# Performance work log

Measured on AMD Instinct MI355X. Metric: run time of the kernel, lower is better.

The kernel has to match this reference:

```python
import jax, jax.numpy as jnp
import numpy as np

TOK, CPC, RHY = 135, 12, 8
HID, STACK, KEY, EMB = 400, 32, 300, 50
B, T = 1, 4096


def setup_inputs() -> dict:
    key = jax.random.key(0)
    ks = jax.random.split(key, 32)
    w = lambda k, shape, s=0.05: jax.random.normal(k, shape, jnp.float32) * s
    inp = {
        'xr': jax.random.randint(ks[0], (B, T), 0, RHY, dtype=jnp.int32),
        'xcpc': jax.random.randint(ks[1], (B, T), 0, CPC, dtype=jnp.int32),
        'xma': jax.random.randint(ks[2], (B, T), 0, TOK, dtype=jnp.int32),
        'emb_midi': w(ks[3], (TOK, EMB)),
        'emb_cpc': w(ks[4], (CPC, EMB)),
        'emb_rhythm': w(ks[5], (RHY, EMB)),
        # note_rnn: 2-layer LSTM, input 3*EMB=150, hidden 400 (torch gate order i,f,g,o)
        'note_Wih0': w(ks[6], (4 * HID, 3 * EMB)),
        'note_Whh0': w(ks[7], (4 * HID, HID)),
        'note_bih0': w(ks[8], (4 * HID,)),
        'note_bhh0': w(ks[9], (4 * HID,)),
        'note_Wih1': w(ks[10], (4 * HID, HID)),
        'note_Whh1': w(ks[11], (4 * HID, HID)),
        'note_bih1': w(ks[12], (4 * HID,)),
        'note_bhh1': w(ks[13], (4 * HID,)),
        'note_fcW': w(ks[14], (3 * EMB, HID)),
        'note_fcb': w(ks[15], (3 * EMB,)),
        # stack memory
        'act_W': w(ks[16], (3, HID)),
        'act_b': w(ks[17], (3,)),
        'D_param': jax.random.normal(ks[18], (1, HID), jnp.float32),
        # key_rnn: 1-layer LSTM, input HID, hidden KEY
        'key_Wih': w(ks[19], (4 * KEY, HID)),
        'key_Whh': w(ks[20], (4 * KEY, KEY)),
        'key_bih': w(ks[21], (4 * KEY,)),
        'key_bhh': w(ks[22], (4 * KEY,)),
        'key_fcW': w(ks[23], (HID, KEY)),
        'key_fcb': w(ks[24], (HID,)),
    }
    return inp


def lstm_layer(x, Wih, Whh, bih, bhh):
    # x: [B,T,I] -> outputs [B,T,H], final (h,c) [B,H]. torch gate order i,f,g,o.
    Bsz = x.shape[0]
    H = Whh.shape[1]
    xg = jnp.einsum('bti,gi->btg', x, Wih) + bih  # precompute input projections

    def step(carry, xt):  # xt: [B,4H]
        h, c = carry
        g = xt + h @ Whh.T + bhh
        i, f, gg, o = jnp.split(g, 4, axis=-1)
        c = jax.nn.sigmoid(f) * c + jax.nn.sigmoid(i) * jnp.tanh(gg)
        h = jax.nn.sigmoid(o) * jnp.tanh(c)
        return (h, c), h

    init = (jnp.zeros((Bsz, H), x.dtype), jnp.zeros((Bsz, H), x.dtype))
    (h, c), hs = jax.lax.scan(step, init, jnp.swapaxes(xg, 0, 1))
    return jnp.swapaxes(hs, 0, 1), h, c


def stack_memory(rnn_out, act_W, act_b, D_param):
    # Per-timestep push/pop/no-op gated stack; returns per-step stack snapshots.
    Bsz, Tlen, H = rnn_out.shape
    probs = jax.nn.softmax(rnn_out @ act_W.T + act_b, axis=-1)            # [B,T,3]
    push_val = jax.nn.sigmoid(jnp.einsum('oh,bth->bt', D_param, rnn_out))  # [B,T]

    def step(s, xs):  # s: [B,STACK,H]
        p, pv = xs  # p: [B,3], pv: [B]
        a = jnp.concatenate([s[:, 1:], s[:, -1:]], axis=1)    # stack[:-1]=stack[1:]
        b = jnp.concatenate([a[:, :1], a[:, :-1]], axis=1)    # stack[1:]=stack[:-1]
        top = p[:, 0:1] * pv[:, None] + p[:, 1:2] * b[:, 1] + p[:, 2:3] * b[:, 0]
        s = b.at[:, 0].set(top)
        return s, s

    init = jnp.zeros((Bsz, STACK, H), rnn_out.dtype)
    _, stacks = jax.lax.scan(step, init, (jnp.swapaxes(probs, 0, 1), push_val.T))
    return jnp.swapaxes(stacks, 0, 1)  # [B,T,STACK,H]


def reference(xr, xcpc, xma, emb_midi, emb_cpc, emb_rhythm,
              note_Wih0, note_Whh0, note_bih0, note_bhh0,
              note_Wih1, note_Whh1, note_bih1, note_bhh1,
              note_fcW, note_fcb, act_W, act_b, D_param,
              key_Wih, key_Whh, key_bih, key_bhh, key_fcW, key_fcb):
    x = jnp.concatenate([emb_midi[xma], emb_cpc[xcpc], emb_rhythm[xr]], axis=2)  # [B,T,150]
    h0, _, _ = lstm_layer(x, note_Wih0, note_Whh0, note_bih0, note_bhh0)
    rnn_out, rh, rc = lstm_layer(h0, note_Wih1, note_Whh1, note_bih1, note_bhh1)
    rtoken_pred = rnn_out @ note_fcW.T + note_fcb  # dropout is identity in eval
    context = stack_memory(rnn_out, act_W, act_b, D_param)  # [B,T,STACK,HID]
    key_in = rh[:, None, :]  # [B,1,HID] (prev_key concat dropped; see notes)
    krnn_out, kh, kc = lstm_layer(key_in, key_Wih, key_Whh, key_bih, key_bhh)
    ktoken_pred = krnn_out @ key_fcW.T + key_fcb  # [B,1,HID]
    return (rtoken_pred, ktoken_pred, context)
```

## Files before the change

kernel.cpp:

```cpp
#include <hip/hip_runtime.h>
#include <stdint.h>

#define T_LEN 4096
#define HID   400
#define G4    1600
#define KDIM  300
#define STACKN 32

__device__ __forceinline__ float fsig(float x){ return 1.f/(1.f + __expf(-x)); }
__device__ __forceinline__ float ftanh(float x){ float e = __expf(2.f*x); return 1.f - 2.f/(e+1.f); }

__device__ __forceinline__ unsigned long long poll_u64(const unsigned long long* src, unsigned tag){
  unsigned long long x0 = __hip_atomic_load(src, __ATOMIC_RELAXED, __HIP_MEMORY_SCOPE_AGENT);
  unsigned long long x1 = __hip_atomic_load(src, __ATOMIC_RELAXED, __HIP_MEMORY_SCOPE_AGENT);
  unsigned long long x2 = __hip_atomic_load(src, __ATOMIC_RELAXED, __HIP_MEMORY_SCOPE_AGENT);
  unsigned long long x3 = __hip_atomic_load(src, __ATOMIC_RELAXED, __HIP_MEMORY_SCOPE_AGENT);
  while ((unsigned)(x0 >> 32) != tag){
    x0 = x1; x1 = x2; x2 = x3;
    x3 = __hip_atomic_load(src, __ATOMIC_RELAXED, __HIP_MEMORY_SCOPE_AGENT);
  }
  return x0;
}
__device__ __forceinline__ float poll_val(const unsigned long long* src, unsigned tag){
  union{unsigned u; float f;} cv; cv.u = (unsigned)poll_u64(src, tag);
  return cv.f;
}

__global__ void __launch_bounds__(256) kgemm0(
    const int* __restrict__ xma, const int* __restrict__ xcpc, const int* __restrict__ xr,
    const float* __restrict__ em, const float* __restrict__ ec, const float* __restrict__ er,
    const float* __restrict__ W, const float* __restrict__ b1, const float* __restrict__ b2,
    float* __restrict__ XG)
{
  __shared__ float xs[8*152];
  const int t0 = blockIdx.x*8;
  const int tid = threadIdx.x;
  for (int idx = tid; idx < 8*150; idx += 256){
    int tt = idx / 150, k = idx - tt*150;
    int t = t0 + tt;
    float v;
    if (k < 50)       v = em[(size_t)xma[t]*50 + k];
    else if (k < 100) v = ec[(size_t)xcpc[t]*50 + (k-50)];
    else              v = er[(size_t)xr[t]*50 + (k-100)];
    xs[tt*152 + k] = v;
  }
  __syncthreads();
  int r = blockIdx.y*256 + tid;
  if (r >= G4) return;
  float acc[8];
  #pragma unroll
  for (int i=0;i<8;i++) acc[i]=0.f;
  const float2* wr = (const float2*)(W + (size_t)r*150);
  for (int k2=0;k2<75;k2++){
    float2 w = wr[k2];
    int k = 2*k2;
    #pragma unroll
    for (int tt=0;tt<8;tt++)
      acc[tt] += w.x*xs[tt*152+k] + w.y*xs[tt*152+k+1];
  }
  float bb = b1[r] + b2[r];
  #pragma unroll
  for (int tt=0;tt<8;tt++)
    XG[(size_t)(t0+tt)*G4 + r] = acc[tt] + bb;
}

__global__ void __launch_bounds__(512,1) kpipe(
    const float* __restrict__ XG0,
    const float* __restrict__ Whh0, const float* __restrict__ Whh1,
    const float* __restrict__ Wih1, const float* __restrict__ bih1,
    const float* __restrict__ bhh1,
    float* __restrict__ RN,
    unsigned long long* hbufA, unsigned long long* hbufB,
    unsigned long long* gbuf, int T)
{
  const int role = blockIdx.x & 7;
  if (role > 2) return;
  const int sub = blockIdx.x >> 3;
  const int tid = threadIdx.x;
  const int row_local = tid >> 2;
  const int part = tid & 3;
  const bool mat = (tid < 400);
  const bool ew  = (tid >= 448 && tid < 473);
  const int  ej  = tid - 448;

  __shared__ float lds_h[HID];
  __shared__ float lds_g[100];

  if (role == 0){
    const int w = sub;
    float wreg[100];
    if (mat){
      int gate = row_local/25, jj = row_local%25;
      int row = gate*400 + w*25 + jj;
      const float4* wr = (const float4*)(Whh0 + (size_t)row*HID) + part*25;
      #pragma unroll
      for (int i=0;i<25;i++){
        float4 v = wr[i];
        wreg[4*i]=v.x; wreg[4*i+1]=v.y; wreg[4*i+2]=v.z; wreg[4*i+3]=v.w;
      }
    }
    const int j = w*25 + ej;
    float c = 0.f;
    for (int t=0; t<T; t++){
      float xgi=0.f, xgf=0.f, xgg=0.f, xgo=0.f;
      unsigned long long th0=0, th1=0, th2=0, th3=0;
      const unsigned long long* thp = 0;
      if (ew){
        const float* xrw = XG0 + (size_t)t*G4;
        xgi = xrw[j]; xgf = xrw[HID+j]; xgg = xrw[2*HID+j]; xgo = xrw[3*HID+j];
        if (t >= 7){
          thp = hbufB + (size_t)((t-6)&7)*HID + j;
          th0 = __hip_atomic_load(thp, __ATOMIC_RELAXED, __HIP_MEMORY_SCOPE_AGENT);
          th1 = __hip_atomic_load(thp, __ATOMIC_RELAXED, __HIP_MEMORY_SCOPE_AGENT);
          th2 = __hip_atomic_load(thp, __ATOMIC_RELAXED, __HIP_MEMORY_SCOPE_AGENT);
          th3 = __hip_atomic_load(thp, __ATOMIC_RELAXED, __HIP_MEMORY_SCOPE_AGENT);
        }
      }
      if (mat){
        float hv = 0.f;
        if (t > 0) hv = poll_val(hbufA + (size_t)(t&7)*HID + tid, (unsigned)t);
        lds_h[tid] = hv;
      }
      __syncthreads();
      float sum = 0.f;
      if (mat){
        const float4* hp = (const float4*)(lds_h + part*100);
        #pragma unroll
        for (int i=0;i<25;i++){
          float4 h4 = hp[i];
          sum += wreg[4*i]*h4.x + wreg[4*i+1]*h4.y + wreg[4*i+2]*h4.z + wreg[4*i+3]*h4.w;
        }
      }
      sum += __shfl_xor(sum, 1);
      sum += __shfl_xor(sum, 2);
      if (mat && part==0) lds_g[row_local] = sum;
      __syncthreads();
      if (ew){
        float gi = xgi + lds_g[ej];
        float gf = xgf + lds_g[25+ej];
        float gg = xgg + lds_g[50+ej];
        float go = xgo + lds_g[75+ej];
        float si = fsig(gi), sf = fsig(gf), so = fsig(go), tg = ftanh(gg);
        c = sf*c + si*tg;
        float h = so*ftanh(c);
        if (t >= 7){
          unsigned want = (unsigned)(t-6);
          while ((unsigned)(th0 >> 32) != want){
            th0 = th1; th1 = th2; th2 = th3;
            th3 = __hip_atomic_load(thp, __ATOMIC_RELAXED, __HIP_MEMORY_SCOPE_AGENT);
          }
        }
        union{unsigned u; float f;} cv; cv.f = h;
        unsigned long long pk = ((unsigned long long)(unsigned)(t+1) << 32) | (unsigned long long)cv.u;
        __hip_atomic_store(hbufA + (size_t)((t+1)&7)*HID + j, pk,
                           __ATOMIC_RELAXED, __HIP_MEMORY_SCOPE_AGENT);
      }
    }
  } else if (role == 1){
    const int f = sub;
    float wreg[100];
    float bias = 0.f;
    int grow = 0;
    if (mat){
      int gate = row_local/25, jj = row_local%25;
      grow = gate*400 + f*25 + jj;
      const float4* wr = (const float4*)(Wih1 + (size_t)grow*HID) + part*25;
      #pragma unroll
      for (int i=0;i<25;i++){
        float4 v = wr[i];
        wreg[4*i]=v.x; wreg[4*i+1]=v.y; wreg[4*i+2]=v.z; wreg[4*i+3]=v.w;
      }
      if (part==0) bias = bih1[grow] + bhh1[grow];
    }
    for (int t=0; t<T; t++){
      if (mat)
        lds_h[tid] = poll_val(hbufA + (size_t)((t+1)&7)*HID + tid, (unsigned)(t+1));
      __syncthreads();
      float sum = 0.f;
      if (mat){
        const float4* hp = (const float4*)(lds_h + part*100);
        #pragma unroll
        for (int i=0;i<25;i++){
          float4 h4 = hp[i];
          sum += wreg[4*i]*h4.x + wreg[4*i+1]*h4.y + wreg[4*i+2]*h4.z + wreg[4*i+3]*h4.w;
        }
      }
      sum += __shfl_xor(sum, 1);
      sum += __shfl_xor(sum, 2);
      if (mat && part==0){
        union{unsigned u; float f;} cv; cv.f = sum + bias;
        unsigned long long pk = ((unsigned long long)(unsigned)(t+1) << 32) | (unsigned long long)cv.u;
        __hip_atomic_store(gbuf + (size_t)((t+1)&7)*G4 + grow, pk,
                           __ATOMIC_RELAXED, __HIP_MEMORY_SCOPE_AGENT);
      }
      __syncthreads();
    }
  } else {
    const int l = sub;
    float wreg[100];
    if (mat){
      int gate = row_local/25, jj = row_local%25;
      int row = gate*400 + l*25 + jj;
      const float4* wr = (const float4*)(Whh1 + (size_t)row*HID) + part*25;
      #pragma unroll
      for (int i=0;i<25;i++){
        float4 v = wr[i];
        wreg[4*i]=v.x; wreg[4*i+1]=v.y; wreg[4*i+2]=v.z; wreg[4*i+3]=v.w;
      }
    }
    const int j = l*25 + ej;
    float c = 0.f;
    for (int t=0; t<T; t++){
      if (mat){
        float hv = 0.f;
        if (t > 0) hv = poll_val(hbufB + (size_t)(t&7)*HID + tid, (unsigned)t);
        lds_h[tid] = hv;
      }
      __syncthreads();
      float xg0=0.f, xg1v=0.f, xg2=0.f, xg3=0.f;
      if (ew){
        const unsigned long long* gb = gbuf + (size_t)((t+1)&7)*G4 + j;
        unsigned want = (unsigned)(t+1);
        unsigned long long v0, v1, v2, v3;
        for (;;){
          v0 = __hip_atomic_load(gb,        __ATOMIC_RELAXED, __HIP_MEMORY_SCOPE_AGENT);
          v1 = __hip_atomic_load(gb + 400,  __ATOMIC_RELAXED, __HIP_MEMORY_SCOPE_AGENT);
          v2 = __hip_atomic_load(gb + 800,  __ATOMIC_RELAXED, __HIP_MEMORY_SCOPE_AGENT);
          v3 = __hip_atomic_load(gb + 1200, __ATOMIC_RELAXED, __HIP_MEMORY_SCOPE_AGENT);
          if (((unsigned)(v0>>32)==want) & ((unsigned)(v1>>32)==want) &
              ((unsigned)(v2>>32)==want) & ((unsigned)(v3>>32)==want)) break;
        }
        union{unsigned u; float f;} c0,c1,c2,c3;
        c0.u=(unsigned)v0; c1.u=(unsigned)v1; c2.u=(unsigned)v2; c3.u=(unsigned)v3;
        xg0=c0.f; xg1v=c1.f; xg2=c2.f; xg3=c3.f;
      }
      float sum = 0.f;
      if (mat){
        const float4* hp = (const float4*)(lds_h + part*100);
        #pragma unroll
        for (int i=0;i<25;i++){
          float4 h4 = hp[i];
          sum += wreg[4*i]*h4.x + wreg[4*i+1]*h4.y + wreg[4*i+2]*h4.z + wreg[4*i+3]*h4.w;
        }
      }
      sum += __shfl_xor(sum, 1);
      sum += __shfl_xor(sum, 2);
      if (mat && part==0) lds_g[row_local] = sum;
      __syncthreads();
      if (ew){
        float gi = xg0  + lds_g[ej];
        float gf = xg1v + lds_g[25+ej];
        float gg = xg2  + lds_g[50+ej];
        float go = xg3  + lds_g[75+ej];
        float si = fsig(gi), sf = fsig(gf), so = fsig(go), tg = ftanh(gg);
        c = sf*c + si*tg;
        float h = so*ftanh(c);
        union{unsigned u; float f;} cv; cv.f = h;
        unsigned long long pk = ((unsigned long long)(unsigned)(t+1) << 32) | (unsigned long long)cv.u;
        __hip_atomic_store(hbufB + (size_t)((t+1)&7)*HID + j, pk,
                           __ATOMIC_RELAXED, __HIP_MEMORY_SCOPE_AGENT);
        RN[(size_t)t*HID + j] = h;
      }
    }
  }
}

__global__ void __launch_bounds__(256) krtoken(
    const float* __restrict__ RN, const float* __restrict__ fcW,
    const float* __restrict__ fcb, float* __restrict__ out)
{
  __shared__ float xs[8*400];
  const int t0 = blockIdx.x*8;
  const int tid = threadIdx.x;
  for (int idx = tid; idx < 8*400; idx += 256)
    xs[idx] = RN[(size_t)t0*400 + idx];
  __syncthreads();
  if (tid >= 150) return;
  float acc[8];
  #pragma unroll
  for (int i=0;i<8;i++) acc[i]=0.f;
  const float4* wr = (const float4*)(fcW + (size_t)tid*400);
  for (int k4=0;k4<100;k4++){
    float4 w = wr[k4];
    #pragma unroll
    for (int tt=0;tt<8;tt++){
      const float4 x4 = *(const float4*)(xs + tt*400 + 4*k4);
      acc[tt] += w.x*x4.x + w.y*x4.y + w.z*x4.z + w.w*x4.w;
    }
  }
  float bb = fcb[tid];
  #pragma unroll
  for (int tt=0;tt<8;tt++)
    out[(size_t)(t0+tt)*150 + tid] = acc[tt] + bb;
}

__global__ void kfinal(const float* __restrict__ RN, const float* __restrict__ actW,
                       const float* __restrict__ actb, const float* __restrict__ Dp,
                       float* __restrict__ vbuf)
{
  int t = blockIdx.x, l = threadIdx.x;
  const float* r = RN + (size_t)t*HID;
  float s0=0.f, s1=0.f, s2=0.f, sd=0.f;
  for (int k=l; k<HID; k+=64){
    float rv = r[k];
    s0 += actW[k]*rv;
    s1 += actW[400+k]*rv;
    s2 += actW[800+k]*rv;
    sd += Dp[k]*rv;
  }
  #pragma unroll
  for (int o=1;o<64;o<<=1){
    s0 += __shfl_xor(s0,o); s1 += __shfl_xor(s1,o);
    s2 += __shfl_xor(s2,o); sd += __shfl_xor(sd,o);
  }
  if (l==0){
    s0 += actb[0]; s1 += actb[1]; s2 += actb[2];
    float m = fmaxf(s0, fmaxf(s1, s2));
    float e0 = __expf(s0-m), e1 = __expf(s1-m), e2 = __expf(s2-m);
    float p0 = e0/(e0+e1+e2);
    vbuf[t] = p0 * fsig(sd);
  }
}

__global__ void kctx(const float* __restrict__ vbuf, uint4* __restrict__ ctx, int n16){
  int i = blockIdx.x*256 + threadIdx.x;
  int stride = gridDim.x*256;
  for (; i<n16; i+=stride){
    int t = i / 3200;
    int p = i - t*3200;
    uint4 z;
    if (p < 100){
      float v = vbuf[t];
      union{float f; uint32_t u;} cv; cv.f = v;
      z.x = z.y = z.z = z.w = cv.u;
    } else {
      z.x = z.y = z.z = z.w = 0u;
    }
    ctx[i] = z;
  }
}

__global__ void __launch_bounds__(512) kkey(
    const float* __restrict__ RN, const float* __restrict__ Wih,
    const float* __restrict__ bih, const float* __restrict__ bhh,
    const float* __restrict__ fcW, const float* __restrict__ fcb,
    float* __restrict__ out)
{
  __shared__ float rh[HID];
  __shared__ float gk[4*KDIM];
  __shared__ float hk[KDIM];
  int tid = threadIdx.x;
  if (tid < HID) rh[tid] = RN[(size_t)(T_LEN-1)*HID + tid];
  __syncthreads();
  for (int r = tid; r < 4*KDIM; r += 512){
    const float4* wr = (const float4*)(Wih + (size_t)r*HID);
    float acc = 0.f;
    for (int k4=0;k4<100;k4++){
      float4 w = wr[k4];
      const float4 x4 = *(const float4*)(rh + 4*k4);
      acc += w.x*x4.x + w.y*x4.y + w.z*x4.z + w.w*x4.w;
    }
    gk[r] = acc + bih[r] + bhh[r];
  }
  __syncthreads();
  if (tid < KDIM){
    float gi = gk[tid], gg = gk[2*KDIM+tid], go = gk[3*KDIM+tid];
    float cc = fsig(gi)*ftanh(gg);
    hk[tid] = fsig(go)*ftanh(cc);
  }
  __syncthreads();
  if (tid < HID){
    const float4* wr = (const float4*)(fcW + (size_t)tid*KDIM);
    float acc = 0.f;
    for (int k4=0;k4<75;k4++){
      float4 w = wr[k4];
      const float4 x4 = *(const float4*)(hk + 4*k4);
      acc += w.x*x4.x + w.y*x4.y + w.z*x4.z + w.w*x4.w;
    }
    out[tid] = acc + fcb[tid];
  }
}

extern "C" void kernel_launch(void* const* d_in, const int* in_sizes, int n_in,
                              void* d_out, int out_size, void* d_ws, size_t ws_size,
                              hipStream_t stream)
{
  (void)in_sizes; (void)n_in; (void)ws_size;
  const int*   xr   = (const int*)d_in[0];
  const int*   xcpc = (const int*)d_in[1];
  const int*   xma  = (const int*)d_in[2];
  const float* em   = (const float*)d_in[3];
  const float* ec   = (const float*)d_in[4];
  const float* er   = (const float*)d_in[5];
  const float* Wih0 = (const float*)d_in[6];
  const float* Whh0 = (const float*)d_in[7];
  const float* bih0 = (const float*)d_in[8];
  const float* bhh0 = (const float*)d_in[9];
  const float* Wih1 = (const float*)d_in[10];
  const float* Whh1 = (const float*)d_in[11];
  const float* bih1 = (const float*)d_in[12];
  const float* bhh1 = (const float*)d_in[13];
  const float* fcW  = (const float*)d_in[14];
  const float* fcb  = (const float*)d_in[15];
  const float* actW = (const float*)d_in[16];
  const float* actb = (const float*)d_in[17];
  const float* Dp   = (const float*)d_in[18];
  const float* kWih = (const float*)d_in[19];
  const float* kbih = (const float*)d_in[21];
  const float* kbhh = (const float*)d_in[22];
  const float* kfcW = (const float*)d_in[23];
  const float* kfcb = (const float*)d_in[24];

  float* vbuf = (float*)d_ws;

  float* out = (float*)d_out;
  char*  ob  = (char*)d_out;
  size_t total = (size_t)out_size * 4;
  float* XG0 = (float*)(ob + total - 26214400);
  float* RN  = (float*)(ob + total - 32768000);
  char*  ctl = ob + total - 32768000 - 262144;
  unsigned long long* hbufA = (unsigned long long*)(ctl);
  unsigned long long* hbufB = (unsigned long long*)(ctl + 25600);
  unsigned long long* gbuf  = (unsigned long long*)(ctl + 51200);

  float* rtok = out;
  float* ktok = out + 614400;
  uint4* ctxp = (uint4*)(ob + 614800u*4u);
  int n16 = (int)((total - 614800u*4u) >> 4);

  dim3 gg(T_LEN/8, 7);
  kgemm0<<<gg,256,0,stream>>>(xma, xcpc, xr, em, ec, er, Wih0, bih0, bhh0, XG0);
  kpipe<<<128,512,0,stream>>>(XG0, Whh0, Whh1, Wih1, bih1, bhh1, RN,
                              hbufA, hbufB, gbuf, T_LEN);
  krtoken<<<T_LEN/8,256,0,stream>>>(RN, fcW, fcb, rtok);
  kkey<<<1,512,0,stream>>>(RN, kWih, kbih, kbhh, kfcW, kfcb, ktok);
  kfinal<<<T_LEN,64,0,stream>>>(RN, actW, actb, Dp, vbuf);
  kctx<<<2048,256,0,stream>>>(vbuf, ctxp, n16);
}
```

Measured before the change: 10.15 ms.

## Place LSTM recurrent blocks on shared XCCs with local-scope polling and deeper rings

The pipelined LSTM kernel now launches many blocks and uses an atomic ticket scheme keyed on the hardware XCC id. This places the layer-0 recurrence and input-projection blocks on one XCC and the layer-1 recurrence blocks on a second, so the per-step hidden-state exchange stays within a shared L2. Polling uses non-temporal loads with occasional workgroup-scope atomics, each block's own hidden slice is reused from LDS, the ring buffers grow from 8 to 32 slots, and a coarse progress counter replaces per-step back-pressure. A large LDS pad limits blocks to one per CU, and a zeroing kernel resets the control words. The aim is lower cross-XCC synchronisation latency on the serial recurrence, at the cost of relying on undocumented XCC placement and cache-coherence behaviour that could hang or read stale data.

After: 9.523 ms. 6.2% less time.

```diff
diff --git a/kernel.cpp b/kernel.cpp
--- a/kernel.cpp
+++ b/kernel.cpp
@@ -5,25 +5,48 @@
 #define HID   400
 #define G4    1600
 #define KDIM  300
-#define STACKN 32
+#define RING  32
 
 __device__ __forceinline__ float fsig(float x){ return 1.f/(1.f + __expf(-x)); }
 __device__ __forceinline__ float ftanh(float x){ float e = __expf(2.f*x); return 1.f - 2.f/(e+1.f); }
 
-__device__ __forceinline__ unsigned long long poll_u64(const unsigned long long* src, unsigned tag){
-  unsigned long long x0 = __hip_atomic_load(src, __ATOMIC_RELAXED, __HIP_MEMORY_SCOPE_AGENT);
-  unsigned long long x1 = __hip_atomic_load(src, __ATOMIC_RELAXED, __HIP_MEMORY_SCOPE_AGENT);
-  unsigned long long x2 = __hip_atomic_load(src, __ATOMIC_RELAXED, __HIP_MEMORY_SCOPE_AGENT);
-  unsigned long long x3 = __hip_atomic_load(src, __ATOMIC_RELAXED, __HIP_MEMORY_SCOPE_AGENT);
-  while ((unsigned)(x0 >> 32) != tag){
-    x0 = x1; x1 = x2; x2 = x3;
-    x3 = __hip_atomic_load(src, __ATOMIC_RELAXED, __HIP_MEMORY_SCOPE_AGENT);
-  }
-  return x0;
-}
-__device__ __forceinline__ float poll_val(const unsigned long long* src, unsigned tag){
-  union{unsigned u; float f;} cv; cv.u = (unsigned)poll_u64(src, tag);
-  return cv.f;
+__device__ __forceinline__ unsigned long long nt_load(const unsigned long long* p){
+  unsigned long long v;
+  asm volatile("global_load_dwordx2 %0, %1, off nt\n"
+               "s_waitcnt vmcnt(0)"
+               : "=v"(v) : "v"(p) : "memory");
+  return v;
+}
+__device__ __forceinline__ float poll_local(unsigned long long* p, unsigned tag){
+  for(;;){
+    #pragma unroll 1
+    for (int k=0;k<12;k++){
+      unsigned long long x = nt_load(p);
+      if ((unsigned)(x >> 32) == tag){
+        union{unsigned u; float f;} c; c.u = (unsigned)x; return c.f;
+      }
+    }
+    #pragma unroll 1
+    for (int k=0;k<4;k++){
+      unsigned long long x = __hip_atomic_fetch_add(p, 0ull, __ATOMIC_RELAXED,
+                                                    __HIP_MEMORY_SCOPE_WORKGROUP);
+      if ((unsigned)(x >> 32) == tag){
+        union{unsigned u; float f;} c; c.u = (unsigned)x; return c.f;
+      }
+    }
+  }
+}
+__device__ __forceinline__ void st_local(unsigned long long* p, unsigned tag, float v){
+  union{unsigned u; float f;} c; c.f = v;
+  *(volatile unsigned long long*)p =
+      ((unsigned long long)tag << 32) | (unsigned long long)c.u;
+}
+
+#define BAR() asm volatile("s_waitcnt lgkmcnt(0)\n\ts_barrier" ::: "memory")
+
+__global__ void kzero(unsigned long long* __restrict__ p, int n){
+  int i = blockIdx.x*256 + threadIdx.x;
+  if (i < n) p[i] = 0ull;
 }
 
 __global__ void __launch_bounds__(256) kgemm0(
@@ -70,21 +93,56 @@
     const float* __restrict__ Wih1, const float* __restrict__ bih1,
     const float* __restrict__ bhh1,
     float* __restrict__ RN,
-    unsigned long long* hbufA, unsigned long long* hbufB,
-    unsigned long long* gbuf, int T)
+    unsigned long long* hA, unsigned long long* hB, unsigned long long* gb,
+    unsigned* ctlw, int T)
 {
-  const int role = blockIdx.x & 7;
-  if (role > 2) return;
-  const int sub = blockIdx.x >> 3;
+  __shared__ int s_role, s_sub;
+  __shared__ float lds_h[HID];
+  __shared__ float lds_g[100];
+  __shared__ float lds_xg[100];
+  __shared__ float lds_hnew[25];
+  __shared__ float lds_pad[25600];
+
+  unsigned xcc;
+  asm volatile("s_getreg_b32 %0, hwreg(HW_REG_XCC_ID)" : "=s"(xcc));
+  if (threadIdx.x == 0){
+    int role = -1, sub = 0;
+    unsigned tk = atomicAdd(ctlw + 0, 1u);
+    if (tk == 0u)
+      __hip_atomic_store(ctlw + 1, (xcc & 0xffu) | 0x100u,
+                         __ATOMIC_RELAXED, __HIP_MEMORY_SCOPE_AGENT);
+    unsigned aw;
+    do { aw = __hip_atomic_load(ctlw + 1, __ATOMIC_RELAXED, __HIP_MEMORY_SCOPE_AGENT); }
+    while (!(aw & 0x100u));
+    if ((aw & 0xffu) == (xcc & 0xffu)){
+      unsigned t2 = atomicAdd(ctlw + 2, 1u);
+      if (t2 < 16u){ role = 0; sub = (int)t2; }
+      else if (t2 < 32u){ role = 1; sub = (int)t2 - 16; }
+    } else {
+      unsigned exp0 = 0u;
+      __hip_atomic_compare_exchange_strong(ctlw + 4, &exp0, (xcc & 0xffu) | 0x100u,
+          __ATOMIC_RELAXED, __ATOMIC_RELAXED, __HIP_MEMORY_SCOPE_AGENT);
+      unsigned bw = __hip_atomic_load(ctlw + 4, __ATOMIC_RELAXED, __HIP_MEMORY_SCOPE_AGENT);
+      if ((bw & 0xffu) == (xcc & 0xffu)){
+        unsigned t3 = atomicAdd(ctlw + 5, 1u);
+        if (t3 < 16u){ role = 2; sub = (int)t3; }
+      }
+    }
+    s_role = role; s_sub = sub;
+  }
+  __syncthreads();
+  const int role = s_role;
+  const int sub  = s_sub;
+  if (role == -7) lds_pad[threadIdx.x] = 1.f;
+  if (role < 0) return;
+
   const int tid = threadIdx.x;
   const int row_local = tid >> 2;
   const int part = tid & 3;
   const bool mat = (tid < 400);
+  const bool gp  = (tid >= 400 && tid < 500);
   const bool ew  = (tid >= 448 && tid < 473);
-  const int  ej  = tid - 448;
-
-  __shared__ float lds_h[HID];
-  __shared__ float lds_g[100];
+  const int  e   = tid - 448;
 
   if (role == 0){
     const int w = sub;
@@ -99,29 +157,81 @@
         wreg[4*i]=v.x; wreg[4*i+1]=v.y; wreg[4*i+2]=v.z; wreg[4*i+3]=v.w;
       }
     }
-    const int j = w*25 + ej;
+    const int j = w*25 + e;
     float c = 0.f;
     for (int t=0; t<T; t++){
-      float xgi=0.f, xgf=0.f, xgg=0.f, xgo=0.f;
-      unsigned long long th0=0, th1=0, th2=0, th3=0;
-      const unsigned long long* thp = 0;
-      if (ew){
-        const float* xrw = XG0 + (size_t)t*G4;
-        xgi = xrw[j]; xgf = xrw[HID+j]; xgg = xrw[2*HID+j]; xgo = xrw[3*HID+j];
-        if (t >= 7){
-          thp = hbufB + (size_t)((t-6)&7)*HID + j;
-          th0 = __hip_atomic_load(thp, __ATOMIC_RELAXED, __HIP_MEMORY_SCOPE_AGENT);
-          th1 = __hip_atomic_load(thp, __ATOMIC_RELAXED, __HIP_MEMORY_SCOPE_AGENT);
-          th2 = __hip_atomic_load(thp, __ATOMIC_RELAXED, __HIP_MEMORY_SCOPE_AGENT);
-          th3 = __hip_atomic_load(thp, __ATOMIC_RELAXED, __HIP_MEMORY_SCOPE_AGENT);
-        }
-      }
       if (mat){
         float hv = 0.f;
-        if (t > 0) hv = poll_val(hbufA + (size_t)(t&7)*HID + tid, (unsigned)t);
+        if (t > 0){
+          if (tid >= w*25 && tid < w*25+25) hv = lds_hnew[tid - w*25];
+          else hv = poll_local(hA + (size_t)(t & (RING-1))*HID + tid, (unsigned)t);
+        }
         lds_h[tid] = hv;
       }
-      __syncthreads();
+      BAR();
+      float sum = 0.f;
+      float xgi=0.f, xgf=0.f, xgg=0.f, xgo=0.f;
+      if (mat){
+        const float4* hp = (const float4*)(lds_h + part*100);
+        #pragma unroll
+        for (int i=0;i<25;i++){
+          float4 h4 = hp[i];
+          sum += wreg[4*i]*h4.x + wreg[4*i+1]*h4.y + wreg[4*i+2]*h4.z + wreg[4*i+3]*h4.w;
+        }
+      } else {
+        if (ew){
+          const float* xrw = XG0 + (size_t)t*G4;
+          xgi = xrw[j]; xgf = xrw[HID+j]; xgg = xrw[2*HID+j]; xgo = xrw[3*HID+j];
+        }
+        if (tid == 448 && t >= 16 && (t & 7) == 0){
+          unsigned want = (unsigned)(t - 8);
+          unsigned v;
+          do { v = __hip_atomic_load(ctlw + 6, __ATOMIC_RELAXED, __HIP_MEMORY_SCOPE_AGENT); }
+          while ((int)(v - want) < 0);
+        }
+      }
+      sum += __shfl_xor(sum, 1);
+      sum += __shfl_xor(sum, 2);
+      if (mat && part==0) lds_g[row_local] = sum;
+      BAR();
+      if (ew){
+        float gi = xgi + lds_g[e];
+        float gf = xgf + lds_g[25+e];
+        float gg = xgg + lds_g[50+e];
+        float go = xgo + lds_g[75+e];
+        float si = fsig(gi), sf = fsig(gf), so = fsig(go), tg = ftanh(gg);
+        c = sf*c + si*tg;
+        float h = so*ftanh(c);
+        lds_hnew[e] = h;
+        st_local(hA + (size_t)((t+1) & (RING-1))*HID + j, (unsigned)(t+1), h);
+      }
+      BAR();
+    }
+  } else if (role == 1){
+    const int f = sub;
+    float wreg[100];
+    float bias = 0.f;
+    int grow = 0;
+    if (mat){
+      int gate = row_local/25, jj = row_local%25;
+      int row = gate*400 + f*25 + jj;
+      const float4* wr = (const float4*)(Wih1 + (size_t)row*HID) + part*25;
+      #pragma unroll
+      for (int i=0;i<25;i++){
+        float4 v = wr[i];
+        wreg[4*i]=v.x; wreg[4*i+1]=v.y; wreg[4*i+2]=v.z; wreg[4*i+3]=v.w;
+      }
+    }
+    if (gp){
+      int p = tid - 400;
+      int gate = p/25, jj = p%25;
+      grow = gate*400 + f*25 + jj;
+      bias = bih1[grow] + bhh1[grow];
+    }
+    for (int t=0; t<T; t++){
+      if (mat)
+        lds_h[tid] = poll_local(hA + (size_t)((t+1) & (RING-1))*HID + tid, (unsigned)(t+1));
+      BAR();
       float sum = 0.f;
       if (mat){
         const float4* hp = (const float4*)(lds_h + part*100);
@@ -134,70 +244,21 @@
       sum += __shfl_xor(sum, 1);
       sum += __shfl_xor(sum, 2);
       if (mat && part==0) lds_g[row_local] = sum;
-      __syncthreads();
-      if (ew){
-        float gi = xgi + lds_g[ej];
-        float gf = xgf + lds_g[25+ej];
-        float gg = xgg + lds_g[50+ej];
-        float go = xgo + lds_g[75+ej];
-        float si = fsig(gi), sf = fsig(gf), so = fsig(go), tg = ftanh(gg);
-        c = sf*c + si*tg;
-        float h = so*ftanh(c);
-        if (t >= 7){
-          unsigned want = (unsigned)(t-6);
-          while ((unsigned)(th0 >> 32) != want){
-            th0 = th1; th1 = th2; th2 = th3;
-            th3 = __hip_atomic_load(thp, __ATOMIC_RELAXED, __HIP_MEMORY_SCOPE_AGENT);
-          }
-        }
-        union{unsigned u; float f;} cv; cv.f = h;
-        unsigned long long pk = ((unsigned long long)(unsigned)(t+1) << 32) | (unsigned long long)cv.u;
-        __hip_atomic_store(hbufA + (size_t)((t+1)&7)*HID + j, pk,
+      BAR();
+      if (gp){
+        int p = tid - 400;
+        union{unsigned u; float f;} cv; cv.f = lds_g[p] + bias;
+        unsigned long long pk =
+            ((unsigned long long)(unsigned)(t+1) << 32) | (unsigned long long)cv.u;
+        __hip_atomic_store(gb + (size_t)((t+1) & (RING-1))*G4 + grow, pk,
                            __ATOMIC_RELAXED, __HIP_MEMORY_SCOPE_AGENT);
       }
-    }
-  } else if (role == 1){
-    const int f = sub;
-    float wreg[100];
-    float bias = 0.f;
-    int grow = 0;
-    if (mat){
-      int gate = row_local/25, jj = row_local%25;
-      grow = gate*400 + f*25 + jj;
-      const float4* wr = (const float4*)(Wih1 + (size_t)grow*HID) + part*25;
-      #pragma unroll
-      for (int i=0;i<25;i++){
-        float4 v = wr[i];
-        wreg[4*i]=v.x; wreg[4*i+1]=v.y; wreg[4*i+2]=v.z; wreg[4*i+3]=v.w;
-      }
-      if (part==0) bias = bih1[grow] + bhh1[grow];
-    }
-    for (int t=0; t<T; t++){
-      if (mat)
-        lds_h[tid] = poll_val(hbufA + (size_t)((t+1)&7)*HID + tid, (unsigned)(t+1));
-      __syncthreads();
-      float sum = 0.f;
-      if (mat){
-        const float4* hp = (const float4*)(lds_h + part*100);
-        #pragma unroll
-        for (int i=0;i<25;i++){
-          float4 h4 = hp[i];
-          sum += wreg[4*i]*h4.x + wreg[4*i+1]*h4.y + wreg[4*i+2]*h4.z + wreg[4*i+3]*h4.w;
-        }
-      }
-      sum += __shfl_xor(sum, 1);
-      sum += __shfl_xor(sum, 2);
-      if (mat && part==0){
-        union{unsigned u; float f;} cv; cv.f = sum + bias;
-        unsigned long long pk = ((unsigned long long)(unsigned)(t+1) << 32) | (unsigned long long)cv.u;
-        __hip_atomic_store(gbuf + (size_t)((t+1)&7)*G4 + grow, pk,
-                           __ATOMIC_RELAXED, __HIP_MEMORY_SCOPE_AGENT);
-      }
-      __syncthreads();
+      BAR();
     }
   } else {
     const int l = sub;
     float wreg[100];
+    int grow = 0;
     if (mat){
       int gate = row_local/25, jj = row_local%25;
       int row = gate*400 + l*25 + jj;
@@ -208,32 +269,23 @@
         wreg[4*i]=v.x; wreg[4*i+1]=v.y; wreg[4*i+2]=v.z; wreg[4*i+3]=v.w;
       }
     }
-    const int j = l*25 + ej;
+    if (gp){
+      int p = tid - 400;
+      int gate = p/25, jj = p%25;
+      grow = gate*400 + l*25 + jj;
+    }
+    const int j = l*25 + e;
     float c = 0.f;
     for (int t=0; t<T; t++){
       if (mat){
         float hv = 0.f;
-        if (t > 0) hv = poll_val(hbufB + (size_t)(t&7)*HID + tid, (unsigned)t);
+        if (t > 0){
+          if (tid >= l*25 && tid < l*25+25) hv = lds_hnew[tid - l*25];
+          else hv = poll_local(hB + (size_t)(t & (RING-1))*HID + tid, (unsigned)t);
+        }
         lds_h[tid] = hv;
       }
-      __syncthreads();
-      float xg0=0.f, xg1v=0.f, xg2=0.f, xg3=0.f;
-      if (ew){
-        const unsigned long long* gb = gbuf + (size_t)((t+1)&7)*G4 + j;
-        unsigned want = (unsigned)(t+1);
-        unsigned long long v0, v1, v2, v3;
-        for (;;){
-          v0 = __hip_atomic_load(gb,        __ATOMIC_RELAXED, __HIP_MEMORY_SCOPE_AGENT);
-          v1 = __hip_atomic_load(gb + 400,  __ATOMIC_RELAXED, __HIP_MEMORY_SCOPE_AGENT);
-          v2 = __hip_atomic_load(gb + 800,  __ATOMIC_RELAXED, __HIP_MEMORY_SCOPE_AGENT);
-          v3 = __hip_atomic_load(gb + 1200, __ATOMIC_RELAXED, __HIP_MEMORY_SCOPE_AGENT);
-          if (((unsigned)(v0>>32)==want) & ((unsigned)(v1>>32)==want) &
-              ((unsigned)(v2>>32)==want) & ((unsigned)(v3>>32)==want)) break;
-        }
-        union{unsigned u; float f;} c0,c1,c2,c3;
-        c0.u=(unsigned)v0; c1.u=(unsigned)v1; c2.u=(unsigned)v2; c3.u=(unsigned)v3;
-        xg0=c0.f; xg1v=c1.f; xg2=c2.f; xg3=c3.f;
-      }
+      BAR();
       float sum = 0.f;
       if (mat){
         const float4* hp = (const float4*)(lds_h + part*100);
@@ -242,25 +294,36 @@
           float4 h4 = hp[i];
           sum += wreg[4*i]*h4.x + wreg[4*i+1]*h4.y + wreg[4*i+2]*h4.z + wreg[4*i+3]*h4.w;
         }
+      } else if (gp){
+        int p = tid - 400;
+        const unsigned long long* src = gb + (size_t)((t+1) & (RING-1))*G4 + grow;
+        unsigned want = (unsigned)(t+1);
+        unsigned long long x;
+        do { x = __hip_atomic_load(src, __ATOMIC_RELAXED, __HIP_MEMORY_SCOPE_AGENT); }
+        while ((unsigned)(x >> 32) != want);
+        union{unsigned u; float f;} cv; cv.u = (unsigned)x;
+        lds_xg[p] = cv.f;
       }
       sum += __shfl_xor(sum, 1);
       sum += __shfl_xor(sum, 2);
       if (mat && part==0) lds_g[row_local] = sum;
-      __syncthreads();
+      BAR();
       if (ew){
-        float gi = xg0  + lds_g[ej];
-        float gf = xg1v + lds_g[25+ej];
-        float gg = xg2  + lds_g[50+ej];
-        float go = xg3  + lds_g[75+ej];
-        float si = fsig(gi), sf = fsig(gf), so = fsig(go), tg = ftanh(gg);
-        c = sf*c + si*tg;
+        float gi = lds_xg[e]    + lds_g[e];
+        float gf = lds_xg[25+e] + lds_g[25+e];
+        float gg = lds_xg[50+e] + lds_g[50+e];
+        float go = lds_xg[75+e] + lds_g[75+e];
+        float si = fsig(gi), sfo = fsig(gf), so = fsig(go), tg = ftanh(gg);
+        c = sfo*c + si*tg;
         float h = so*ftanh(c);
-        union{unsigned u; float f;} cv; cv.f = h;
-        unsigned long long pk = ((unsigned long long)(unsigned)(t+1) << 32) | (unsigned long long)cv.u;
-        __hip_atomic_store(hbufB + (size_t)((t+1)&7)*HID + j, pk,
-                           __ATOMIC_RELAXED, __HIP_MEMORY_SCOPE_AGENT);
+        lds_hnew[e] = h;
+        st_local(hB + (size_t)((t+1) & (RING-1))*HID + j, (unsigned)(t+1), h);
         RN[(size_t)t*HID + j] = h;
-      }
+        if (tid == 448 && (t & 7) == 0)
+          __hip_atomic_store(ctlw + 6, (unsigned)t,
+                             __ATOMIC_RELAXED, __HIP_MEMORY_SCOPE_AGENT);
+      }
+      BAR();
     }
   }
 }
@@ -418,10 +481,12 @@
   size_t total = (size_t)out_size * 4;
   float* XG0 = (float*)(ob + total - 26214400);
   float* RN  = (float*)(ob + total - 32768000);
-  char*  ctl = ob + total - 32768000 - 262144;
-  unsigned long long* hbufA = (unsigned long long*)(ctl);
-  unsigned long long* hbufB = (unsigned long long*)(ctl + 25600);
-  unsigned long long* gbuf  = (unsigned long long*)(ctl + 51200);
+  char*  ctl = ob + total - 32768000 - 1048576;
+  unsigned*           ctlw = (unsigned*)(ctl);
+  unsigned long long* hAb  = (unsigned long long*)(ctl + 4096);
+  unsigned long long* hBb  = (unsigned long long*)(ctl + 4096 + 102400);
+  unsigned long long* gbb  = (unsigned long long*)(ctl + 4096 + 204800);
+  int nz = (4096 + 204800 + 409600) / 8;
 
   float* rtok = out;
   float* ktok = out + 614400;
@@ -429,9 +494,10 @@
   int n16 = (int)((total - 614800u*4u) >> 4);
 
   dim3 gg(T_LEN/8, 7);
+  kzero<<<(nz+255)/256,256,0,stream>>>((unsigned long long*)ctl, nz);
   kgemm0<<<gg,256,0,stream>>>(xma, xcpc, xr, em, ec, er, Wih0, bih0, bhh0, XG0);
-  kpipe<<<128,512,0,stream>>>(XG0, Whh0, Whh1, Wih1, bih1, bhh1, RN,
-                              hbufA, hbufB, gbuf, T_LEN);
+  kpipe<<<2048,512,0,stream>>>(XG0, Whh0, Whh1, Wih1, bih1, bhh1, RN,
+                               hAb, hBb, gbb, ctlw, T_LEN);
   krtoken<<<T_LEN/8,256,0,stream>>>(RN, fcW, fcb, rtok);
   kkey<<<1,512,0,stream>>>(RN, kWih, kbih, kbhh, kfcW, kfcb, ktok);
   kfinal<<<T_LEN,64,0,stream>>>(RN, actW, actb, Dp, vbuf);
```
